# Performance work log

Hardware: AMD Instinct MI355X
Metric: run time of the kernel (lower is better)

## Reference

```python
import jax, jax.numpy as jnp
import numpy as np

B, C, T, H, W = 2, 512, 8, 16, 16
NUM_HEADS = 8
HEAD_DIM = C // NUM_HEADS


def setup_inputs() -> dict:
    key = jax.random.key(0)
    ks = jax.random.split(key, 6)
    x = jax.random.normal(ks[0], (B, C, T, H, W), dtype=jnp.float32)
    # LayerNorm params
    ln_w = jnp.ones((C,), dtype=jnp.float32)
    ln_b = jnp.zeros((C,), dtype=jnp.float32)
    # 1x1x1 Conv3d == per-token linear; weight stored [out, in]
    w_qkv = jax.random.normal(ks[1], (3 * C, C), dtype=jnp.float32) * (1.0 / np.sqrt(C))
    b_qkv = jnp.zeros((3 * C,), dtype=jnp.float32)
    w_proj = jax.random.normal(ks[2], (C, C), dtype=jnp.float32) * (1.0 / np.sqrt(C))
    b_proj = jnp.zeros((C,), dtype=jnp.float32)
    return {"x": x, "ln_w": ln_w, "ln_b": ln_b, "w_qkv": w_qkv,
            "b_qkv": b_qkv, "w_proj": w_proj, "b_proj": b_proj}


def reference(x, ln_w, ln_b, w_qkv, b_qkv, w_proj, b_proj):
    Bx, Cx, Tx, Hx, Wx = x.shape
    N = Tx * Hx * Wx
    scale = HEAD_DIM ** -0.5

    # [B,C,T,H,W] -> [B,N,C]
    x_flat = jnp.transpose(x, (0, 2, 3, 4, 1)).reshape(Bx, N, Cx)

    # LayerNorm over channels
    mu = jnp.mean(x_flat, axis=-1, keepdims=True)
    var = jnp.var(x_flat, axis=-1, keepdims=True)
    x_flat = (x_flat - mu) * jax.lax.rsqrt(var + 1e-5) * ln_w + ln_b

    # QKV (1x1x1 conv == linear). Output channel layout: [3, heads, head_dim]
    qkv = jnp.einsum('bnc,oc->bno', x_flat, w_qkv) + b_qkv  # [B,N,3C]
    qkv = qkv.reshape(Bx, N, 3, NUM_HEADS, HEAD_DIM)
    qkv = jnp.transpose(qkv, (2, 0, 3, 1, 4))  # [3,B,heads,N,head_dim]
    q, k, v = qkv[0], qkv[1], qkv[2]

    attn = jnp.einsum('bhnd,bhmd->bhnm', q, k) * scale
    attn = jax.nn.softmax(attn, axis=-1)
    x_attn = jnp.einsum('bhnm,bhmd->bhnd', attn, v)  # [B,heads,N,head_dim]
    x_attn = jnp.transpose(x_attn, (0, 2, 1, 3)).reshape(Bx, N, Cx)

    # proj (1x1x1 conv == linear)
    x_attn = jnp.einsum('bnc,oc->bno', x_attn, w_proj) + b_proj

    # NOTE: residual is on the *normalized* x_flat (as in the original module)
    x_out = x_flat + x_attn
    x_out = x_out.reshape(Bx, Tx, Hx, Wx, Cx)
    return jnp.transpose(x_out, (0, 4, 1, 2, 3))  # [B,C,T,H,W]
```

## Files before the change

kernel.cpp:

```cpp
#include <hip/hip_runtime.h>
#include <hip/hip_bf16.h>

#define BB 2
#define CC 512
#define NN 2048
#define NHEADS 8
#define HDIM 64
#define NSPLIT 2
#define KVQ 1024

typedef __attribute__((ext_vector_type(8))) __bf16 bf16x8;
typedef __attribute__((ext_vector_type(4))) __bf16 bf16x4;
typedef __attribute__((ext_vector_type(4))) float f32x4;

typedef const __attribute__((address_space(1))) unsigned int guint;
typedef __attribute__((address_space(3))) unsigned int suint;

#define QSCALE 0.18033688f
#define MX3(a, b, c) fmaxf(fmaxf(a, b), c)

__global__ __launch_bounds__(256) void cvt_w_kernel(
    const float* __restrict__ wqkv, const float* __restrict__ wproj,
    __bf16* __restrict__ wqkv_bf, __bf16* __restrict__ wproj_bf) {
  int i = blockIdx.x * 256 + threadIdx.x;
  const int NQ = 3 * CC * CC / 4;
  if (i < NQ) {
    float4 v = *(const float4*)&wqkv[(size_t)i * 4];
    bf16x4 pk = {(__bf16)v.x, (__bf16)v.y, (__bf16)v.z, (__bf16)v.w};
    *(bf16x4*)&wqkv_bf[(size_t)i * 4] = pk;
  } else {
    int j = i - NQ;
    float4 v = *(const float4*)&wproj[(size_t)j * 4];
    bf16x4 pk = {(__bf16)v.x, (__bf16)v.y, (__bf16)v.z, (__bf16)v.w};
    *(bf16x4*)&wproj_bf[(size_t)j * 4] = pk;
  }
}

__global__ __launch_bounds__(256) void ln_fused_kernel(
    const float* __restrict__ x, const float* __restrict__ lnw,
    const float* __restrict__ lnb, float* __restrict__ mu,
    float* __restrict__ rstd, __bf16* __restrict__ xln_t) {
  __shared__ float Xs[512][20];
  __shared__ float rs[16][17];
  __shared__ float rq[16][17];
  __shared__ float mloc[16];
  __shared__ float rloc[16];
  int bid = blockIdx.x;
  int n_tile = 2 * (((bid >> 4) << 3) + (bid & 7)) + ((bid >> 3) & 1);
  int n0 = n_tile * 16;
  int b = blockIdx.y;
  int tid = threadIdx.x;
#pragma unroll
  for (int l = 0; l < 8; ++l) {
    int e = tid + 256 * l;
    int row = e >> 2, quad = e & 3;
    float4 v = *(const float4*)&x[((size_t)b * CC + row) * NN + n0 + quad * 4];
    *(float4*)&Xs[row][quad * 4] = v;
  }
  __syncthreads();
  {
    int tk = tid & 15, part = tid >> 4;
    float s = 0.f, ss = 0.f;
    int c0 = part * 32;
#pragma unroll 8
    for (int j = 0; j < 32; ++j) {
      float v = Xs[c0 + j][tk];
      s += v;
      ss += v * v;
    }
    rs[part][tk] = s;
    rq[part][tk] = ss;
  }
  __syncthreads();
  if (tid < 16) {
    float S = 0.f, SS = 0.f;
#pragma unroll
    for (int p = 0; p < 16; ++p) {
      S += rs[p][tid];
      SS += rq[p][tid];
    }
    float m = S * (1.0f / CC);
    float var = SS * (1.0f / CC) - m * m;
    float rv = rsqrtf(var + 1e-5f);
    mloc[tid] = m;
    rloc[tid] = rv;
    int tok = b * NN + n0 + tid;
    mu[tok] = m;
    rstd[tok] = rv;
  }
  __syncthreads();
  {
    int tk = tid >> 4;
    int cseg = (tid & 15) * 32;
    float mun = mloc[tk], rsn = rloc[tk];
    __bf16 outv[32];
#pragma unroll
    for (int j = 0; j < 32; ++j) {
      int c = cseg + j;
      outv[j] = (__bf16)((Xs[c][tk] - mun) * rsn * lnw[c] + lnb[c]);
    }
    __bf16* dst = &xln_t[((size_t)b * NN + n0 + tk) * CC + cseg];
#pragma unroll
    for (int q = 0; q < 4; ++q) *(bf16x8*)&dst[q * 8] = *(bf16x8*)&outv[q * 8];
  }
}

__global__ __launch_bounds__(256, 3) void qkv_mfma_kernel(
    const __bf16* __restrict__ xln_t, const __bf16* __restrict__ wbf,
    const float* __restrict__ bias, __bf16* __restrict__ qt,
    __bf16* __restrict__ kt, __bf16* __restrict__ vbf) {
  __shared__ __align__(16) __bf16 As[2][64][64];
  __shared__ __align__(16) __bf16 Bs[2][128][64];
  int n0 = blockIdx.x * 128;
  bool swap = blockIdx.y < 16;
  int m0 = swap ? blockIdx.y * 64 : 1024 + ((int)blockIdx.y - 16) * 64;
  int b = blockIdx.z;
  int tid = threadIdx.x;
  int wid = tid >> 6, lane = tid & 63;
  int g = lane >> 4, c = lane & 15;
  int wr = wid >> 1, wc = wid & 1;
  const __bf16* xln = xln_t + (size_t)b * NN * CC;
  int l7 = lane & 7, l3 = lane >> 3;
  int xr = (l7 ^ l3) * 8;
  auto STAGE = [&](int buf, int k0) {
#pragma unroll
    for (int j = 0; j < 2; ++j) {
      int r = wid * 16 + 8 * j + l3;
      __builtin_amdgcn_global_load_lds(
          (guint*)(wbf + (size_t)(m0 + r) * CC + k0 + xr),
          (suint*)&As[buf][wid * 16 + 8 * j][0], 16, 0, 0);
    }
#pragma unroll
    for (int j = 0; j < 4; ++j) {
      int r = wid * 32 + 8 * j + l3;
      __builtin_amdgcn_global_load_lds(
          (guint*)(xln + (size_t)(n0 + r) * CC + k0 + xr),
          (suint*)&Bs[buf][wid * 32 + 8 * j][0], 16, 0, 0);
    }
  };
  STAGE(0, 0);
  f32x4 acc[2][4] = {};
  int cxor = c & 7;
  for (int ks = 0; ks < 8; ++ks) {
    int cur = ks & 1;
    if (ks < 7) {
      STAGE(cur ^ 1, (ks + 1) * 64);
      asm volatile("s_waitcnt vmcnt(6)" ::: "memory");
    } else {
      asm volatile("s_waitcnt vmcnt(0)" ::: "memory");
    }
    __builtin_amdgcn_sched_barrier(0);
    __builtin_amdgcn_s_barrier();
    __builtin_amdgcn_s_setprio(1);
#pragma unroll
    for (int hh = 0; hh < 2; ++hh) {
      int ch = ((hh * 4 + g) ^ cxor) * 8;
      bf16x8 af[2], bfr[4];
#pragma unroll
      for (int mi = 0; mi < 2; ++mi)
        af[mi] = *(const bf16x8*)&As[cur][wr * 32 + mi * 16 + c][ch];
#pragma unroll
      for (int nj = 0; nj < 4; ++nj)
        bfr[nj] = *(const bf16x8*)&Bs[cur][wc * 64 + nj * 16 + c][ch];
      if (swap) {
#pragma unroll
        for (int mi = 0; mi < 2; ++mi)
#pragma unroll
          for (int nj = 0; nj < 4; ++nj)
            acc[mi][nj] = __builtin_amdgcn_mfma_f32_16x16x32_bf16(
                bfr[nj], af[mi], acc[mi][nj], 0, 0, 0);
      } else {
#pragma unroll
        for (int mi = 0; mi < 2; ++mi)
#pragma unroll
          for (int nj = 0; nj < 4; ++nj)
            acc[mi][nj] = __builtin_amdgcn_mfma_f32_16x16x32_bf16(
                af[mi], bfr[nj], acc[mi][nj], 0, 0, 0);
      }
    }
    __builtin_amdgcn_s_setprio(0);
    __builtin_amdgcn_s_barrier();
  }
  if (swap) {
    int obase = m0 + wr * 32;
    int sec = obase >> 9;
    int osec = obase & 511;
    int head = osec >> 6;
    int dbase = osec & 63;
    __bf16* dst = (sec == 0 ? qt : kt) + (size_t)(b * NHEADS + head) * NN * HDIM;
    float scl = (sec == 0) ? QSCALE : 1.0f;
#pragma unroll
    for (int mi = 0; mi < 2; ++mi) {
      float bo = bias[obase + mi * 16 + c];
      int d = dbase + mi * 16 + c;
#pragma unroll
      for (int nj = 0; nj < 4; ++nj)
#pragma unroll
        for (int r = 0; r < 4; ++r) {
          int n = n0 + wc * 64 + nj * 16 + 4 * g + r;
          dst[(size_t)n * HDIM + d] = (__bf16)((acc[mi][nj][r] + bo) * scl);
        }
    }
  } else {
#pragma unroll
    for (int mi = 0; mi < 2; ++mi)
#pragma unroll
      for (int r = 0; r < 4; ++r) {
        int o = m0 + wr * 32 + mi * 16 + 4 * g + r;
        int ch = o - 1024;
        float bo = bias[o];
#pragma unroll
        for (int nj = 0; nj < 4; ++nj) {
          int n = n0 + wc * 64 + nj * 16 + c;
          vbf[((size_t)b * CC + ch) * NN + n] = (__bf16)(acc[mi][nj][r] + bo);
        }
      }
  }
}

__global__ __launch_bounds__(256, 3) void attn_mfma_kernel(
    const __bf16* __restrict__ qt, const __bf16* __restrict__ ktg,
    const __bf16* __restrict__ vbf, __bf16* __restrict__ opart,
    float* __restrict__ ml) {
  __shared__ __align__(16) __bf16 Kb[2][64][64];
  __shared__ __align__(16) __bf16 Vb[2][64][64];
  int tid = threadIdx.x;
  int wid = tid >> 6, lane = tid & 63;
  int g = lane >> 4, c = lane & 15;
  int n0 = blockIdx.x * 128;
  int h = blockIdx.y;
  int b = blockIdx.z >> 1, split = blockIdx.z & 1;
  int bh = b * NHEADS + h;
  const __bf16* qbase = qt + ((size_t)bh * NN + n0) * HDIM;
  const __bf16* kbase = ktg + ((size_t)bh * NN + split * KVQ) * HDIM;
  const __bf16* vbase = vbf + ((size_t)b * CC + h * HDIM) * NN + split * KVQ;

  int l7 = lane & 7, l3 = lane >> 3;
  int xr = (l7 ^ l3) * 8;
  auto STAGE = [&](int buf, int mt) {
#pragma unroll
    for (int j = 0; j < 2; ++j) {
      int r = wid * 16 + 8 * j + l3;
      int gr = (r & 0x20) | (((r >> 2) & 3) << 3) | (((r >> 4) & 1) << 2) | (r & 3);
      const __bf16* ksrc = kbase + (size_t)(mt + gr) * HDIM + xr;
      __builtin_amdgcn_global_load_lds((guint*)ksrc,
                                       (suint*)&Kb[buf][wid * 16 + 8 * j][0],
                                       16, 0, 0);
      const __bf16* vsrc = vbase + (size_t)r * NN + mt + xr;
      __builtin_amdgcn_global_load_lds((guint*)vsrc,
                                       (suint*)&Vb[buf][wid * 16 + 8 * j][0],
                                       16, 0, 0);
    }
  };

  STAGE(0, 0);
  bf16x8 aq[2][2];
#pragma unroll
  for (int qg = 0; qg < 2; ++qg) {
    const __bf16* qp = qbase + (size_t)(wid * 32 + qg * 16 + c) * HDIM;
    aq[qg][0] = *(const bf16x8*)(qp + g * 8);
    aq[qg][1] = *(const bf16x8*)(qp + 32 + g * 8);
  }
  f32x4 O[2][4] = {};
  f32x4 Ol[2] = {};
  float m_[2] = {-1e30f, -1e30f};
  int cxor = (c & 7);
  const bf16x8 vones = {(__bf16)1.f, (__bf16)1.f, (__bf16)1.f, (__bf16)1.f,
                        (__bf16)1.f, (__bf16)1.f, (__bf16)1.f, (__bf16)1.f};

  for (int t = 0; t < KVQ / 64; ++t) {
    int cur = t & 1;
    if (t + 1 < KVQ / 64) {
      STAGE(cur ^ 1, (t + 1) * 64);
      asm volatile("s_waitcnt vmcnt(4)" ::: "memory");
    } else {
      asm volatile("s_waitcnt vmcnt(0)" ::: "memory");
    }
    __builtin_amdgcn_sched_barrier(0);
    __builtin_amdgcn_s_barrier();
    f32x4 st[2][4];
    __builtin_amdgcn_s_setprio(1);
#pragma unroll
    for (int t4 = 0; t4 < 4; ++t4) {
      bf16x8 bk0 = *(const bf16x8*)&Kb[cur][t4 * 16 + c][(g ^ cxor) * 8];
      bf16x8 bk1 = *(const bf16x8*)&Kb[cur][t4 * 16 + c][((4 + g) ^ cxor) * 8];
#pragma unroll
      for (int qg = 0; qg < 2; ++qg) {
        f32x4 acc = {0.f, 0.f, 0.f, 0.f};
        acc = __builtin_amdgcn_mfma_f32_16x16x32_bf16(bk0, aq[qg][0], acc, 0, 0, 0);
        acc = __builtin_amdgcn_mfma_f32_16x16x32_bf16(bk1, aq[qg][1], acc, 0, 0, 0);
        st[qg][t4] = acc;
      }
    }
    __builtin_amdgcn_s_setprio(0);
    bf16x8 pa[2][2];
#pragma unroll
    for (int qg = 0; qg < 2; ++qg) {
      float g0 = MX3(st[qg][0][0], st[qg][0][1], st[qg][0][2]);
      float g1 = MX3(st[qg][0][3], st[qg][1][0], st[qg][1][1]);
      float g2 = MX3(st[qg][1][2], st[qg][1][3], st[qg][2][0]);
      float g3 = MX3(st[qg][2][1], st[qg][2][2], st[qg][2][3]);
      float g4 = MX3(st[qg][3][0], st[qg][3][1], st[qg][3][2]);
      float pm = fmaxf(MX3(g0, g1, g2), MX3(g3, g4, st[qg][3][3]));
      if (!__all(pm <= m_[qg] + 8.0f)) {
        float rm = fmaxf(pm, __shfl_xor(pm, 16));
        rm = fmaxf(rm, __shfl_xor(rm, 32));
        float mn = fmaxf(m_[qg], rm);
        float fs = exp2f(m_[qg] - mn);
        m_[qg] = mn;
#pragma unroll
        for (int dt = 0; dt < 4; ++dt)
#pragma unroll
          for (int r = 0; r < 4; ++r) O[qg][dt][r] *= fs;
#pragma unroll
        for (int r = 0; r < 4; ++r) Ol[qg][r] *= fs;
      }
#pragma unroll
      for (int t4 = 0; t4 < 4; ++t4) {
        float p0 = exp2f(st[qg][t4][0] - m_[qg]);
        float p1 = exp2f(st[qg][t4][1] - m_[qg]);
        float p2 = exp2f(st[qg][t4][2] - m_[qg]);
        float p3 = exp2f(st[qg][t4][3] - m_[qg]);
        bf16x8* pp = &pa[qg][t4 >> 1];
        int o4 = (t4 & 1) * 4;
        (*pp)[o4 + 0] = (__bf16)p0;
        (*pp)[o4 + 1] = (__bf16)p1;
        (*pp)[o4 + 2] = (__bf16)p2;
        (*pp)[o4 + 3] = (__bf16)p3;
      }
    }
    __builtin_amdgcn_s_setprio(1);
#pragma unroll
    for (int dt = 0; dt < 4; ++dt) {
      bf16x8 bv0 = *(const bf16x8*)&Vb[cur][dt * 16 + c][(g ^ cxor) * 8];
      bf16x8 bv1 = *(const bf16x8*)&Vb[cur][dt * 16 + c][((4 + g) ^ cxor) * 8];
#pragma unroll
      for (int qg = 0; qg < 2; ++qg) {
        O[qg][dt] = __builtin_amdgcn_mfma_f32_16x16x32_bf16(bv0, pa[qg][0],
                                                            O[qg][dt], 0, 0, 0);
        O[qg][dt] = __builtin_amdgcn_mfma_f32_16x16x32_bf16(bv1, pa[qg][1],
                                                            O[qg][dt], 0, 0, 0);
      }
    }
#pragma unroll
    for (int qg = 0; qg < 2; ++qg) {
      Ol[qg] = __builtin_amdgcn_mfma_f32_16x16x32_bf16(vones, pa[qg][0],
                                                       Ol[qg], 0, 0, 0);
      Ol[qg] = __builtin_amdgcn_mfma_f32_16x16x32_bf16(vones, pa[qg][1],
                                                       Ol[qg], 0, 0, 0);
    }
    __builtin_amdgcn_s_setprio(0);
    __builtin_amdgcn_s_barrier();
  }
#pragma unroll
  for (int qg = 0; qg < 2; ++qg) {
    size_t prow = ((size_t)(split * BB + b) * NHEADS + h) * NN +
                  (n0 + wid * 32 + qg * 16 + c);
#pragma unroll
    for (int dt = 0; dt < 4; ++dt) {
      bf16x4 pk = {(__bf16)O[qg][dt][0], (__bf16)O[qg][dt][1],
                   (__bf16)O[qg][dt][2], (__bf16)O[qg][dt][3]};
      *(bf16x4*)&opart[prow * HDIM + dt * 16 + 4 * g] = pk;
    }
    if (lane < 16) {
      float2 mlv = {m_[qg], Ol[qg][0]};
      *(float2*)&ml[prow * 2] = mlv;
    }
  }
}

__global__ __launch_bounds__(256) void attn_combine_kernel(
    const __bf16* __restrict__ opart, const float* __restrict__ ml,
    __bf16* __restrict__ xa_t) {
  int t = threadIdx.x;
  int row_local = t >> 4;
  int dq = (t & 15) * 4;
  int R = blockIdx.x * 16 + row_local;
  int n = R & (NN - 1);
  int bh = R >> 11;
  int b = bh >> 3, h = bh & 7;
  size_t ps[NSPLIT];
  float ms[NSPLIT], ls[NSPLIT];
  float m = -1e30f;
#pragma unroll
  for (int s = 0; s < NSPLIT; ++s) {
    ps[s] = ((size_t)(s * BB + b) * NHEADS + h) * NN + n;
    ms[s] = ml[ps[s] * 2];
    ls[s] = ml[ps[s] * 2 + 1];
    m = fmaxf(m, ms[s]);
  }
  float lsum = 0.f;
  float ws[NSPLIT];
#pragma unroll
  for (int s = 0; s < NSPLIT; ++s) {
    ws[s] = exp2f(ms[s] - m);
    lsum += ls[s] * ws[s];
  }
  float linv = 1.0f / lsum;
  float acc[4] = {0.f, 0.f, 0.f, 0.f};
#pragma unroll
  for (int s = 0; s < NSPLIT; ++s) {
    bf16x4 ov = *(const bf16x4*)&opart[ps[s] * HDIM + dq];
#pragma unroll
    for (int j = 0; j < 4; ++j) acc[j] += (float)ov[j] * ws[s];
  }
  bf16x4 pk = {(__bf16)(acc[0] * linv), (__bf16)(acc[1] * linv),
               (__bf16)(acc[2] * linv), (__bf16)(acc[3] * linv)};
  *(bf16x4*)&xa_t[((size_t)b * NN + n) * CC + h * HDIM + dq] = pk;
}

__global__ __launch_bounds__(256, 4) void proj_mfma_kernel(
    const __bf16* __restrict__ xa_t, const __bf16* __restrict__ wbf,
    const float* __restrict__ bias, const float* __restrict__ x,
    const float* __restrict__ mu, const float* __restrict__ rstd,
    const float* __restrict__ lnw, const float* __restrict__ lnb,
    float* __restrict__ out) {
  __shared__ __align__(16) __bf16 As[2][64][64];
  __shared__ __align__(16) __bf16 Bs[2][64][64];
  int n0 = blockIdx.x * 64;
  int m0 = blockIdx.y * 64;
  int b = blockIdx.z;
  int tid = threadIdx.x;
  int wid = tid >> 6, lane = tid & 63;
  int g = lane >> 4, c = lane & 15;
  int wr = wid >> 1, wc = wid & 1;
  const __bf16* xab = xa_t + (size_t)b * NN * CC;
  int l7 = lane & 7, l3 = lane >> 3;
  int xr = (l7 ^ l3) * 8;
  auto STAGE = [&](int buf, int k0) {
#pragma unroll
    for (int j = 0; j < 2; ++j) {
      int r = wid * 16 + 8 * j + l3;
      __builtin_amdgcn_global_load_lds(
          (guint*)(wbf + (size_t)(m0 + r) * CC + k0 + xr),
          (suint*)&As[buf][wid * 16 + 8 * j][0], 16, 0, 0);
      __builtin_amdgcn_global_load_lds(
          (guint*)(xab + (size_t)(n0 + r) * CC + k0 + xr),
          (suint*)&Bs[buf][wid * 16 + 8 * j][0], 16, 0, 0);
    }
  };
  STAGE(0, 0);
  f32x4 acc[2][2] = {};
  int cxor = c & 7;
  for (int ks = 0; ks < 8; ++ks) {
    int cur = ks & 1;
    if (ks < 7) {
      STAGE(cur ^ 1, (ks + 1) * 64);
      asm volatile("s_waitcnt vmcnt(4)" ::: "memory");
    } else {
      asm volatile("s_waitcnt vmcnt(0)" ::: "memory");
    }
    __builtin_amdgcn_sched_barrier(0);
    __builtin_amdgcn_s_barrier();
    __builtin_amdgcn_s_setprio(1);
#pragma unroll
    for (int hh = 0; hh < 2; ++hh) {
      int ch = ((hh * 4 + g) ^ cxor) * 8;
      bf16x8 af[2], bfr[2];
#pragma unroll
      for (int mi = 0; mi < 2; ++mi)
        af[mi] = *(const bf16x8*)&As[cur][wr * 32 + mi * 16 + c][ch];
#pragma unroll
      for (int nj = 0; nj < 2; ++nj)
        bfr[nj] = *(const bf16x8*)&Bs[cur][wc * 32 + nj * 16 + c][ch];
#pragma unroll
      for (int mi = 0; mi < 2; ++mi)
#pragma unroll
        for (int nj = 0; nj < 2; ++nj)
          acc[mi][nj] = __builtin_amdgcn_mfma_f32_16x16x32_bf16(
              af[mi], bfr[nj], acc[mi][nj], 0, 0, 0);
    }
    __builtin_amdgcn_s_setprio(0);
    __builtin_amdgcn_s_barrier();
  }
#pragma unroll
  for (int mi = 0; mi < 2; ++mi)
#pragma unroll
    for (int r = 0; r < 4; ++r) {
      int o = m0 + wr * 32 + mi * 16 + 4 * g + r;
      float bo = bias[o], gw = lnw[o], gb = lnb[o];
#pragma unroll
      for (int nj = 0; nj < 2; ++nj) {
        int n = n0 + wc * 32 + nj * 16 + c;
        int tok = b * NN + n;
        float xv = x[((size_t)b * CC + o) * NN + n];
        float xlnv = (xv - mu[tok]) * rstd[tok] * gw + gb;
        out[((size_t)b * CC + o) * NN + n] = acc[mi][nj][r] + bo + xlnv;
      }
    }
}

extern "C" void kernel_launch(void* const* d_in, const int* in_sizes, int n_in,
                              void* d_out, int out_size, void* d_ws, size_t ws_size,
                              hipStream_t stream) {
  const float* x = (const float*)d_in[0];
  const float* lnw = (const float*)d_in[1];
  const float* lnb = (const float*)d_in[2];
  const float* wqkv = (const float*)d_in[3];
  const float* bqkv = (const float*)d_in[4];
  const float* wproj = (const float*)d_in[5];
  const float* bproj = (const float*)d_in[6];
  float* out = (float*)d_out;
  (void)in_sizes; (void)n_in; (void)out_size; (void)ws_size;

  char* wsb = (char*)d_ws;
  float* mu = (float*)wsb;
  float* rstd = mu + 4096;
  const size_t HSZ = (size_t)BB * NHEADS * NN * HDIM;
  __bf16* qt = (__bf16*)(wsb + 32768);
  __bf16* kt = qt + HSZ;
  __bf16* vbf = kt + HSZ;
  __bf16* xa_t = vbf + HSZ;
  __bf16* xln_t = xa_t + HSZ;
  __bf16* opart = xln_t + HSZ;
  float* ml = (float*)(opart + (size_t)NSPLIT * HSZ);
  __bf16* wqkv_bf = (__bf16*)((char*)ml + 524288);
  __bf16* wproj_bf = wqkv_bf + (size_t)3 * CC * CC;

  hipLaunchKernelGGL(cvt_w_kernel, dim3(1024), dim3(256), 0, stream,
                     wqkv, wproj, wqkv_bf, wproj_bf);
  hipLaunchKernelGGL(ln_fused_kernel, dim3(128, 2), dim3(256), 0, stream,
                     x, lnw, lnb, mu, rstd, xln_t);
  hipLaunchKernelGGL(qkv_mfma_kernel, dim3(16, 24, 2), dim3(256), 0, stream,
                     xln_t, wqkv_bf, bqkv, qt, kt, vbf);
  hipLaunchKernelGGL(attn_mfma_kernel, dim3(16, 8, BB * NSPLIT), dim3(256), 0,
                     stream, qt, kt, vbf, opart, ml);
  hipLaunchKernelGGL(attn_combine_kernel, dim3(2048), dim3(256), 0, stream,
                     opart, ml, xa_t);
  hipLaunchKernelGGL(proj_mfma_kernel, dim3(32, 8, 2), dim3(256), 0, stream,
                     xa_t, wproj_bf, bproj, x, mu, rstd, lnw, lnb, out);
}
```

Before: 76.14 us.

## Fuse LN with weight conversion and fold split-KV combine into proj GEMM

The weight-conversion kernel is merged into the LayerNorm kernel as extra blocks in one flat grid, which removes a launch. The attention split-combine kernel is removed. The projection GEMM now loads both partial outputs and their max/sum values, merges them in registers and writes the combined bf16 tile into swizzled LDS for its B operand. This drops the xa_t round trip through memory and one more launch. In exchange, the proj kernel repeats the combine work for each of the 8 m-blocks, and its B staging now goes through registers with a full vmcnt(0) wait, which weakens the load/compute overlap.

```diff
diff --git a/kernel.cpp b/kernel.cpp
--- a/kernel.cpp
+++ b/kernel.cpp
@@ -19,37 +19,37 @@
 #define QSCALE 0.18033688f
 #define MX3(a, b, c) fmaxf(fmaxf(a, b), c)
 
-__global__ __launch_bounds__(256) void cvt_w_kernel(
-    const float* __restrict__ wqkv, const float* __restrict__ wproj,
+__global__ __launch_bounds__(256) void ln_cvt_kernel(
+    const float* __restrict__ x, const float* __restrict__ lnw,
+    const float* __restrict__ lnb, const float* __restrict__ wqkv,
+    const float* __restrict__ wproj, float* __restrict__ mu,
+    float* __restrict__ rstd, __bf16* __restrict__ xln_t,
     __bf16* __restrict__ wqkv_bf, __bf16* __restrict__ wproj_bf) {
-  int i = blockIdx.x * 256 + threadIdx.x;
-  const int NQ = 3 * CC * CC / 4;
-  if (i < NQ) {
-    float4 v = *(const float4*)&wqkv[(size_t)i * 4];
-    bf16x4 pk = {(__bf16)v.x, (__bf16)v.y, (__bf16)v.z, (__bf16)v.w};
-    *(bf16x4*)&wqkv_bf[(size_t)i * 4] = pk;
-  } else {
-    int j = i - NQ;
-    float4 v = *(const float4*)&wproj[(size_t)j * 4];
-    bf16x4 pk = {(__bf16)v.x, (__bf16)v.y, (__bf16)v.z, (__bf16)v.w};
-    *(bf16x4*)&wproj_bf[(size_t)j * 4] = pk;
-  }
-}
-
-__global__ __launch_bounds__(256) void ln_fused_kernel(
-    const float* __restrict__ x, const float* __restrict__ lnw,
-    const float* __restrict__ lnb, float* __restrict__ mu,
-    float* __restrict__ rstd, __bf16* __restrict__ xln_t) {
   __shared__ float Xs[512][20];
   __shared__ float rs[16][17];
   __shared__ float rq[16][17];
   __shared__ float mloc[16];
   __shared__ float rloc[16];
-  int bid = blockIdx.x;
+  int tid = threadIdx.x;
+  if (blockIdx.x >= 256) {
+    int i = (blockIdx.x - 256) * 256 + tid;
+    const int NQ = 3 * CC * CC / 4;
+    if (i < NQ) {
+      float4 v = *(const float4*)&wqkv[(size_t)i * 4];
+      bf16x4 pk = {(__bf16)v.x, (__bf16)v.y, (__bf16)v.z, (__bf16)v.w};
+      *(bf16x4*)&wqkv_bf[(size_t)i * 4] = pk;
+    } else {
+      int j = i - NQ;
+      float4 v = *(const float4*)&wproj[(size_t)j * 4];
+      bf16x4 pk = {(__bf16)v.x, (__bf16)v.y, (__bf16)v.z, (__bf16)v.w};
+      *(bf16x4*)&wproj_bf[(size_t)j * 4] = pk;
+    }
+    return;
+  }
+  int bid = blockIdx.x & 127;
+  int b = blockIdx.x >> 7;
   int n_tile = 2 * (((bid >> 4) << 3) + (bid & 7)) + ((bid >> 3) & 1);
   int n0 = n_tile * 16;
-  int b = blockIdx.y;
-  int tid = threadIdx.x;
 #pragma unroll
   for (int l = 0; l < 8; ++l) {
     int e = tid + 256 * l;
@@ -369,52 +369,12 @@
   }
 }
 
-__global__ __launch_bounds__(256) void attn_combine_kernel(
+__global__ __launch_bounds__(256, 4) void proj_fused_kernel(
     const __bf16* __restrict__ opart, const float* __restrict__ ml,
-    __bf16* __restrict__ xa_t) {
-  int t = threadIdx.x;
-  int row_local = t >> 4;
-  int dq = (t & 15) * 4;
-  int R = blockIdx.x * 16 + row_local;
-  int n = R & (NN - 1);
-  int bh = R >> 11;
-  int b = bh >> 3, h = bh & 7;
-  size_t ps[NSPLIT];
-  float ms[NSPLIT], ls[NSPLIT];
-  float m = -1e30f;
-#pragma unroll
-  for (int s = 0; s < NSPLIT; ++s) {
-    ps[s] = ((size_t)(s * BB + b) * NHEADS + h) * NN + n;
-    ms[s] = ml[ps[s] * 2];
-    ls[s] = ml[ps[s] * 2 + 1];
-    m = fmaxf(m, ms[s]);
-  }
-  float lsum = 0.f;
-  float ws[NSPLIT];
-#pragma unroll
-  for (int s = 0; s < NSPLIT; ++s) {
-    ws[s] = exp2f(ms[s] - m);
-    lsum += ls[s] * ws[s];
-  }
-  float linv = 1.0f / lsum;
-  float acc[4] = {0.f, 0.f, 0.f, 0.f};
-#pragma unroll
-  for (int s = 0; s < NSPLIT; ++s) {
-    bf16x4 ov = *(const bf16x4*)&opart[ps[s] * HDIM + dq];
-#pragma unroll
-    for (int j = 0; j < 4; ++j) acc[j] += (float)ov[j] * ws[s];
-  }
-  bf16x4 pk = {(__bf16)(acc[0] * linv), (__bf16)(acc[1] * linv),
-               (__bf16)(acc[2] * linv), (__bf16)(acc[3] * linv)};
-  *(bf16x4*)&xa_t[((size_t)b * NN + n) * CC + h * HDIM + dq] = pk;
-}
-
-__global__ __launch_bounds__(256, 4) void proj_mfma_kernel(
-    const __bf16* __restrict__ xa_t, const __bf16* __restrict__ wbf,
-    const float* __restrict__ bias, const float* __restrict__ x,
-    const float* __restrict__ mu, const float* __restrict__ rstd,
-    const float* __restrict__ lnw, const float* __restrict__ lnb,
-    float* __restrict__ out) {
+    const __bf16* __restrict__ wbf, const float* __restrict__ bias,
+    const float* __restrict__ x, const float* __restrict__ mu,
+    const float* __restrict__ rstd, const float* __restrict__ lnw,
+    const float* __restrict__ lnb, float* __restrict__ out) {
   __shared__ __align__(16) __bf16 As[2][64][64];
   __shared__ __align__(16) __bf16 Bs[2][64][64];
   int n0 = blockIdx.x * 64;
@@ -424,34 +384,62 @@
   int wid = tid >> 6, lane = tid & 63;
   int g = lane >> 4, c = lane & 15;
   int wr = wid >> 1, wc = wid & 1;
-  const __bf16* xab = xa_t + (size_t)b * NN * CC;
   int l7 = lane & 7, l3 = lane >> 3;
   int xr = (l7 ^ l3) * 8;
-  auto STAGE = [&](int buf, int k0) {
+  auto STAGE_A = [&](int buf, int k0) {
 #pragma unroll
     for (int j = 0; j < 2; ++j) {
       int r = wid * 16 + 8 * j + l3;
       __builtin_amdgcn_global_load_lds(
           (guint*)(wbf + (size_t)(m0 + r) * CC + k0 + xr),
           (suint*)&As[buf][wid * 16 + 8 * j][0], 16, 0, 0);
-      __builtin_amdgcn_global_load_lds(
-          (guint*)(xab + (size_t)(n0 + r) * CC + k0 + xr),
-          (suint*)&Bs[buf][wid * 16 + 8 * j][0], 16, 0, 0);
     }
   };
-  STAGE(0, 0);
+  int rB = tid >> 2, qB = tid & 3;
+  bf16x8 b0[2], b1[2];
+  float2 ml0, ml1;
+  auto LOAD_B = [&](int h) {
+    size_t p0 = ((size_t)(0 * BB + b) * NHEADS + h) * NN + n0 + rB;
+    size_t p1 = ((size_t)(1 * BB + b) * NHEADS + h) * NN + n0 + rB;
+    b0[0] = *(const bf16x8*)&opart[p0 * HDIM + qB * 16];
+    b0[1] = *(const bf16x8*)&opart[p0 * HDIM + qB * 16 + 8];
+    b1[0] = *(const bf16x8*)&opart[p1 * HDIM + qB * 16];
+    b1[1] = *(const bf16x8*)&opart[p1 * HDIM + qB * 16 + 8];
+    ml0 = *(const float2*)&ml[p0 * 2];
+    ml1 = *(const float2*)&ml[p1 * 2];
+  };
+  auto WRITE_B = [&](int buf) {
+    float mm = fmaxf(ml0.x, ml1.x);
+    float w0 = exp2f(ml0.x - mm), w1 = exp2f(ml1.x - mm);
+    float linv = 1.0f / (ml0.y * w0 + ml1.y * w1);
+    w0 *= linv;
+    w1 *= linv;
+#pragma unroll
+    for (int ch = 0; ch < 2; ++ch) {
+      __bf16 ov[8];
+#pragma unroll
+      for (int j = 0; j < 8; ++j)
+        ov[j] = (__bf16)((float)b0[ch][j] * w0 + (float)b1[ch][j] * w1);
+      int chunk = (qB * 2 + ch) ^ (rB & 7);
+      *(bf16x8*)&Bs[buf][rB][chunk * 8] = *(bf16x8*)&ov;
+    }
+  };
+
+  LOAD_B(0);
+  STAGE_A(0, 0);
+  asm volatile("s_waitcnt vmcnt(0)" ::: "memory");
+  __builtin_amdgcn_sched_barrier(0);
+  WRITE_B(0);
+  __syncthreads();
+
   f32x4 acc[2][2] = {};
   int cxor = c & 7;
   for (int ks = 0; ks < 8; ++ks) {
     int cur = ks & 1;
     if (ks < 7) {
-      STAGE(cur ^ 1, (ks + 1) * 64);
-      asm volatile("s_waitcnt vmcnt(4)" ::: "memory");
-    } else {
-      asm volatile("s_waitcnt vmcnt(0)" ::: "memory");
-    }
-    __builtin_amdgcn_sched_barrier(0);
-    __builtin_amdgcn_s_barrier();
+      STAGE_A(cur ^ 1, (ks + 1) * 64);
+      LOAD_B(ks + 1);
+    }
     __builtin_amdgcn_s_setprio(1);
 #pragma unroll
     for (int hh = 0; hh < 2; ++hh) {
@@ -471,6 +459,13 @@
               af[mi], bfr[nj], acc[mi][nj], 0, 0, 0);
     }
     __builtin_amdgcn_s_setprio(0);
+    __builtin_amdgcn_s_barrier();
+    if (ks < 7) {
+      asm volatile("s_waitcnt vmcnt(0)" ::: "memory");
+      __builtin_amdgcn_sched_barrier(0);
+      WRITE_B(cur ^ 1);
+      asm volatile("s_waitcnt lgkmcnt(0)" ::: "memory");
+    }
     __builtin_amdgcn_s_barrier();
   }
 #pragma unroll
@@ -510,23 +505,19 @@
   __bf16* qt = (__bf16*)(wsb + 32768);
   __bf16* kt = qt + HSZ;
   __bf16* vbf = kt + HSZ;
-  __bf16* xa_t = vbf + HSZ;
-  __bf16* xln_t = xa_t + HSZ;
+  __bf16* xln_t = vbf + HSZ;
   __bf16* opart = xln_t + HSZ;
   float* ml = (float*)(opart + (size_t)NSPLIT * HSZ);
   __bf16* wqkv_bf = (__bf16*)((char*)ml + 524288);
   __bf16* wproj_bf = wqkv_bf + (size_t)3 * CC * CC;
 
-  hipLaunchKernelGGL(cvt_w_kernel, dim3(1024), dim3(256), 0, stream,
-                     wqkv, wproj, wqkv_bf, wproj_bf);
-  hipLaunchKernelGGL(ln_fused_kernel, dim3(128, 2), dim3(256), 0, stream,
-                     x, lnw, lnb, mu, rstd, xln_t);
+  hipLaunchKernelGGL(ln_cvt_kernel, dim3(1280), dim3(256), 0, stream,
+                     x, lnw, lnb, wqkv, wproj, mu, rstd, xln_t, wqkv_bf,
+                     wproj_bf);
   hipLaunchKernelGGL(qkv_mfma_kernel, dim3(16, 24, 2), dim3(256), 0, stream,
                      xln_t, wqkv_bf, bqkv, qt, kt, vbf);
   hipLaunchKernelGGL(attn_mfma_kernel, dim3(16, 8, BB * NSPLIT), dim3(256), 0,
                      stream, qt, kt, vbf, opart, ml);
-  hipLaunchKernelGGL(attn_combine_kernel, dim3(2048), dim3(256), 0, stream,
-                     opart, ml, xa_t);
-  hipLaunchKernelGGL(proj_mfma_kernel, dim3(32, 8, 2), dim3(256), 0, stream,
-                     xa_t, wproj_bf, bproj, x, mu, rstd, lnw, lnb, out);
+  hipLaunchKernelGGL(proj_fused_kernel, dim3(32, 8, 2), dim3(256), 0, stream,
+                     opart, ml, wproj_bf, bproj, x, mu, rstd, lnw, lnb, out);
 }
```

Result: faster. 71.67 us, median of 2 (-5.9%).
